# Performance work log

Measured on AMD Instinct MI355X. Metric: run time of the kernel, lower is better.

## Reference

```python
import jax, jax.numpy as jnp
import numpy as np

BATCH = 32768
NUM_CLASSES = 1000

def setup_inputs() -> dict:
    key = jax.random.key(0)
    k1, k2 = jax.random.split(key)
    input = jax.random.normal(k1, (BATCH, NUM_CLASSES), dtype=jnp.float32)
    target = jax.random.randint(k2, (BATCH, NUM_CLASSES), 0, 2, dtype=jnp.int32)
    return {"input": input, "target": target}

def reference(input, target):
    # LSEP: loss = log(1 + sum_{i} sum_{p in pos_i} sum_{n in neg_i} exp(x[i,n] - x[i,p]))
    # The pair sum factorizes per sample:
    #   sum_{p,n} exp(x_n - x_p) = (sum_{n in neg} exp(x_n)) * (sum_{p in pos} exp(-x_p))
    pos = target > 0
    neg = target == 0
    s_neg = jnp.sum(jnp.where(neg, jnp.exp(input), 0.0), axis=1)   # [B]
    s_pos = jnp.sum(jnp.where(pos, jnp.exp(-input), 0.0), axis=1)  # [B]
    total = jnp.sum(s_neg * s_pos)
    return jnp.log1p(total).reshape(1).astype(jnp.float32)
```

## Files before the change

kernel.cpp:

```cpp
#include <hip/hip_runtime.h>
#include <math.h>

#define BATCH 32768
#define NCLS 1000
#define NC4  250

__global__ __launch_bounds__(256) void lsep_row_kernel(
    const float* __restrict__ x,
    const int*   __restrict__ t,
    float* __restrict__ row_out) {

    const int row = blockIdx.x;
    const int tid = threadIdx.x;

    const float4* xr = (const float4*)(x + (size_t)row * NCLS);
    const int4*   tr = (const int4*)(t + (size_t)row * NCLS);

    float sn = 0.0f, sp = 0.0f;
    if (tid < NC4) {
        float4 xv = xr[tid];
        int4   tv = tr[tid];
        if (tv.x == 0) sn += __expf(xv.x); else sp += __expf(-xv.x);
        if (tv.y == 0) sn += __expf(xv.y); else sp += __expf(-xv.y);
        if (tv.z == 0) sn += __expf(xv.z); else sp += __expf(-xv.z);
        if (tv.w == 0) sn += __expf(xv.w); else sp += __expf(-xv.w);
    }

    #pragma unroll
    for (int off = 32; off > 0; off >>= 1) {
        sn += __shfl_down(sn, off, 64);
        sp += __shfl_down(sp, off, 64);
    }

    __shared__ float ssn[4], ssp[4];
    const int wave = tid >> 6;
    const int lane = tid & 63;
    if (lane == 0) { ssn[wave] = sn; ssp[wave] = sp; }
    __syncthreads();

    if (tid == 0) {
        float tn = ssn[0] + ssn[1] + ssn[2] + ssn[3];
        float tp = ssp[0] + ssp[1] + ssp[2] + ssp[3];
        row_out[row] = tn * tp;
    }
}

__global__ __launch_bounds__(256) void lsep_reduce_kernel(
    const float* __restrict__ row_out,
    float* __restrict__ out) {

    const int tid = threadIdx.x;
    float v = 0.0f;
    const float4* r4 = (const float4*)row_out;
    for (int i = tid; i < BATCH / 4; i += 256) {
        float4 a = r4[i];
        v += a.x + a.y + a.z + a.w;
    }

    #pragma unroll
    for (int off = 32; off > 0; off >>= 1)
        v += __shfl_down(v, off, 64);

    __shared__ float sv[4];
    const int wave = tid >> 6;
    const int lane = tid & 63;
    if (lane == 0) sv[wave] = v;
    __syncthreads();

    if (tid == 0) {
        float total = sv[0] + sv[1] + sv[2] + sv[3];
        out[0] = log1pf(total);
    }
}

extern "C" void kernel_launch(void* const* d_in, const int* in_sizes, int n_in,
                              void* d_out, int out_size, void* d_ws, size_t ws_size,
                              hipStream_t stream) {
    const float* x = (const float*)d_in[0];
    const int*   t = (const int*)d_in[1];
    float* out     = (float*)d_out;
    float* row_ws  = (float*)d_ws;

    lsep_row_kernel<<<BATCH, 256, 0, stream>>>(x, t, row_ws);
    lsep_reduce_kernel<<<1, 256, 0, stream>>>(row_ws, out);
}
```

Before: 272.8 us.

## Map one wave per row with multiple rows per wave in persistent grid

Replaces one-block-per-row with a grid of 2048 blocks where each wave processes several rows, reducing each row with wave shuffles only and accumulating per-wave partials. This removes the LDS barrier and the per-row block scheduling overhead, and lets more loads be in flight per wave. exp(-x) is computed as a fast reciprocal of exp(x), and the final reduction reads 8192 per-wave partials. The reciprocal may introduce slight precision differences.

```diff
diff --git a/kernel.cpp b/kernel.cpp
--- a/kernel.cpp
+++ b/kernel.cpp
@@ -1,61 +1,84 @@
 #include <hip/hip_runtime.h>
 #include <math.h>
 
-#define BATCH 32768
-#define NCLS 1000
-#define NC4  250
+#define BATCH   32768
+#define NCLS    1000
+#define NC4     250
+#define NBLOCKS 2048
+#define NWAVES  (NBLOCKS * 4)
 
 __global__ __launch_bounds__(256) void lsep_row_kernel(
     const float* __restrict__ x,
     const int*   __restrict__ t,
-    float* __restrict__ row_out) {
+    float* __restrict__ wave_out) {
 
-    const int row = blockIdx.x;
-    const int tid = threadIdx.x;
+    const int tid   = threadIdx.x;
+    const int lane  = tid & 63;
+    const int gwave = blockIdx.x * 4 + (tid >> 6);
 
-    const float4* xr = (const float4*)(x + (size_t)row * NCLS);
-    const int4*   tr = (const int4*)(t + (size_t)row * NCLS);
+    float acc = 0.0f;
 
-    float sn = 0.0f, sp = 0.0f;
-    if (tid < NC4) {
-        float4 xv = xr[tid];
-        int4   tv = tr[tid];
-        if (tv.x == 0) sn += __expf(xv.x); else sp += __expf(-xv.x);
-        if (tv.y == 0) sn += __expf(xv.y); else sp += __expf(-xv.y);
-        if (tv.z == 0) sn += __expf(xv.z); else sp += __expf(-xv.z);
-        if (tv.w == 0) sn += __expf(xv.w); else sp += __expf(-xv.w);
+    #pragma unroll
+    for (int r = 0; r < BATCH / NWAVES; ++r) {
+        const int row = gwave + r * NWAVES;
+        const float4* xr = (const float4*)(x + (size_t)row * NCLS);
+        const int4*   tr = (const int4*)(t + (size_t)row * NCLS);
+
+        float4 xv[4];
+        int4   tv[4];
+        #pragma unroll
+        for (int j = 0; j < 4; ++j) {
+            const int idx = lane + 64 * j;
+            if (idx < NC4) {
+                xv[j] = xr[idx];
+                tv[j] = tr[idx];
+            }
+        }
+
+        float sn = 0.0f, sp = 0.0f;
+        #pragma unroll
+        for (int j = 0; j < 4; ++j) {
+            const int idx = lane + 64 * j;
+            if (idx < NC4) {
+                {   float e = __expf(xv[j].x); float r1 = __builtin_amdgcn_rcpf(e);
+                    if (tv[j].x == 0) sn += e; else sp += r1; }
+                {   float e = __expf(xv[j].y); float r1 = __builtin_amdgcn_rcpf(e);
+                    if (tv[j].y == 0) sn += e; else sp += r1; }
+                {   float e = __expf(xv[j].z); float r1 = __builtin_amdgcn_rcpf(e);
+                    if (tv[j].z == 0) sn += e; else sp += r1; }
+                {   float e = __expf(xv[j].w); float r1 = __builtin_amdgcn_rcpf(e);
+                    if (tv[j].w == 0) sn += e; else sp += r1; }
+            }
+        }
+
+        #pragma unroll
+        for (int off = 32; off > 0; off >>= 1) {
+            sn += __shfl_down(sn, off, 64);
+            sp += __shfl_down(sp, off, 64);
+        }
+
+        if (lane == 0) acc += sn * sp;
     }
 
-    #pragma unroll
-    for (int off = 32; off > 0; off >>= 1) {
-        sn += __shfl_down(sn, off, 64);
-        sp += __shfl_down(sp, off, 64);
-    }
-
-    __shared__ float ssn[4], ssp[4];
-    const int wave = tid >> 6;
-    const int lane = tid & 63;
-    if (lane == 0) { ssn[wave] = sn; ssp[wave] = sp; }
-    __syncthreads();
-
-    if (tid == 0) {
-        float tn = ssn[0] + ssn[1] + ssn[2] + ssn[3];
-        float tp = ssp[0] + ssp[1] + ssp[2] + ssp[3];
-        row_out[row] = tn * tp;
-    }
+    if (lane == 0) wave_out[gwave] = acc;
 }
 
 __global__ __launch_bounds__(256) void lsep_reduce_kernel(
-    const float* __restrict__ row_out,
+    const float* __restrict__ wave_out,
     float* __restrict__ out) {
 
     const int tid = threadIdx.x;
+    const float4* r4 = (const float4*)wave_out;
+
+    float4 a[8];
+    #pragma unroll
+    for (int j = 0; j < 8; ++j)
+        a[j] = r4[tid + 256 * j];
+
     float v = 0.0f;
-    const float4* r4 = (const float4*)row_out;
-    for (int i = tid; i < BATCH / 4; i += 256) {
-        float4 a = r4[i];
-        v += a.x + a.y + a.z + a.w;
-    }
+    #pragma unroll
+    for (int j = 0; j < 8; ++j)
+        v += (a[j].x + a[j].y) + (a[j].z + a[j].w);
 
     #pragma unroll
     for (int off = 32; off > 0; off >>= 1)
@@ -68,7 +91,7 @@
     __syncthreads();
 
     if (tid == 0) {
-        float total = sv[0] + sv[1] + sv[2] + sv[3];
+        float total = (sv[0] + sv[1]) + (sv[2] + sv[3]);
         out[0] = log1pf(total);
     }
 }
@@ -79,8 +102,8 @@
     const float* x = (const float*)d_in[0];
     const int*   t = (const int*)d_in[1];
     float* out     = (float*)d_out;
-    float* row_ws  = (float*)d_ws;
+    float* wave_ws = (float*)d_ws;
 
-    lsep_row_kernel<<<BATCH, 256, 0, stream>>>(x, t, row_ws);
-    lsep_reduce_kernel<<<1, 256, 0, stream>>>(row_ws, out);
+    lsep_row_kernel<<<NBLOCKS, 256, 0, stream>>>(x, t, wave_ws);
+    lsep_reduce_kernel<<<1, 256, 0, stream>>>(wave_ws, out);
 }
```

Result: no change. 270.1 us (-1.0%).
